# Kernel optimization log

Measured on AMD Instinct MI355X. Metric: run time of the kernel, lower is better.

## Reference

```python
import jax, jax.numpy as jnp
import numpy as np

N = 10000      # nodes
E = 320000     # edges (before self-loops)
IN = 128       # input features
HID = 32       # hidden channels per head
HEADS = 8
OUT = 40       # classes
NEG_SLOPE = 0.2  # PyG GATConv leaky_relu slope


def gat_conv(x, W, a_src, a_dst, b, src, dst, n, concat):
    """One PyG-style GATConv (eval mode, self-loops already in src/dst)."""
    H, C = a_src.shape
    xp = (x @ W).reshape(n, H, C)                       # [N,H,C]
    al_s = jnp.einsum('nhc,hc->nh', xp, a_src)          # [N,H]
    al_d = jnp.einsum('nhc,hc->nh', xp, a_dst)          # [N,H]
    e = jax.nn.leaky_relu(al_s[src] + al_d[dst], NEG_SLOPE)  # [E,H]
    # segment softmax over incoming edges of each dst node
    m = jax.ops.segment_max(e, dst, num_segments=n)
    ee = jnp.exp(e - m[dst])
    s = jax.ops.segment_sum(ee, dst, num_segments=n)
    alpha = ee / (s[dst] + 1e-16)                       # [E,H]
    out = jax.ops.segment_sum(alpha[:, :, None] * xp[src], dst, num_segments=n)  # [N,H,C]
    out = out.reshape(n, H * C) if concat else out.mean(axis=1)
    return out + b


def setup_inputs() -> dict:
    key = jax.random.key(0)
    ks = jax.random.split(key, 16)
    p = lambda k, shape: (jax.random.normal(k, shape, jnp.float32) * 0.1)
    HC = HEADS * HID
    return {
        'x': jax.random.normal(ks[0], (N, IN), jnp.float32),
        'edge_index': jax.random.randint(ks[1], (2, E), 0, N),
        'W1': p(ks[2], (IN, HC)), 'a_src1': p(ks[3], (HEADS, HID)), 'a_dst1': p(ks[4], (HEADS, HID)), 'b1': jnp.zeros((HC,), jnp.float32),
        'W2': p(ks[5], (HC, HC)), 'a_src2': p(ks[6], (HEADS, HID)), 'a_dst2': p(ks[7], (HEADS, HID)), 'b2': jnp.zeros((HC,), jnp.float32),
        'W3': p(ks[8], (HC, OUT)), 'a_src3': p(ks[9], (1, OUT)), 'a_dst3': p(ks[10], (1, OUT)), 'b3': jnp.zeros((OUT,), jnp.float32),
    }


def reference(x, edge_index, W1, a_src1, a_dst1, b1, W2, a_src2, a_dst2, b2,
              W3, a_src3, a_dst3, b3):
    n = x.shape[0]
    loop = jnp.arange(n, dtype=edge_index.dtype)
    src = jnp.concatenate([edge_index[0], loop])   # PyG add_self_loops=True
    dst = jnp.concatenate([edge_index[1], loop])
    h = jax.nn.elu(gat_conv(x, W1, a_src1, a_dst1, b1, src, dst, n, True))
    h = jax.nn.elu(gat_conv(h, W2, a_src2, a_dst2, b2, src, dst, n, True))
    h = gat_conv(h, W3, a_src3, a_dst3, b3, src, dst, n, False)
    return jax.nn.log_softmax(h, axis=1)
```

## Files before the change

kernel.cpp:

```cpp
#include <hip/hip_runtime.h>
#include <hip/hip_bf16.h>
#include <math.h>


#define DEV_INLINE __device__ __forceinline__

typedef __attribute__((ext_vector_type(8))) short short8;
typedef __attribute__((ext_vector_type(4))) float f32x4;
typedef unsigned short ushort_t;
typedef unsigned int uint_t;

#define ELLW 128

DEV_INLINE float leaky02(float x) { return x > 0.f ? x : 0.2f * x; }
DEV_INLINE float elu1(float x) { return x > 0.f ? x : expm1f(x); }

DEV_INLINE ushort_t f2bf(float f) {
    uint_t u = __float_as_uint(f);
    u += 0x7FFFu + ((u >> 16) & 1u);
    return (ushort_t)(u >> 16);
}
DEV_INLINE float bf2f(ushort_t u) { return __uint_as_float(((uint_t)u) << 16); }


DEV_INLINE void prep_body(int i,
                          const float* __restrict__ x, ushort_t* __restrict__ x_bf,
                          const float* __restrict__ W1, ushort_t* __restrict__ W1T,
                          const float* __restrict__ W2, ushort_t* __restrict__ W2T,
                          const float* __restrict__ W3, ushort_t* __restrict__ W3T,
                          const float* __restrict__ as1, const float* __restrict__ ad1,
                          const float* __restrict__ as2, const float* __restrict__ ad2,
                          const float* __restrict__ as3, const float* __restrict__ ad3,
                          int n) {
    int xcnt = n * 32;
    if (i < xcnt) {
        float4 v = *(const float4*)(x + (size_t)i * 4);
        ushort4 o;
        o.x = f2bf(v.x); o.y = f2bf(v.y); o.z = f2bf(v.z); o.w = f2bf(v.w);
        *(ushort4*)(x_bf + (size_t)i * 4) = o;
        return;
    }
    i -= xcnt;
    if (i < 128 * 256) {
        int k = i >> 8, c = i & 255;
        W1T[(size_t)c * 128 + k] = f2bf(W1[i]);
        return;
    }
    i -= 128 * 256;
    if (i < 256 * 256) {
        int k = i >> 8, c = i & 255;
        W2T[(size_t)c * 256 + k] = f2bf(W2[i]);
        return;
    }
    i -= 256 * 256;
    if (i < 256 * 40) {
        int k = i / 40, c = i - k * 40;
        W3T[(size_t)c * 256 + k] = f2bf(W3[i]);
        return;
    }
    i -= 256 * 40;
    if (i < 1024) {
        int h = i >> 7, k = i & 127;
        float acc = 0.f;
#pragma unroll
        for (int c = 0; c < 32; ++c) acc += W1[k * 256 + h * 32 + c] * as1[h * 32 + c];
        W1T[(size_t)(256 + h) * 128 + k] = f2bf(acc);
        return;
    }
    i -= 1024;
    if (i < 1024) {
        int h = i >> 7, k = i & 127;
        float acc = 0.f;
#pragma unroll
        for (int c = 0; c < 32; ++c) acc += W1[k * 256 + h * 32 + c] * ad1[h * 32 + c];
        W1T[(size_t)(264 + h) * 128 + k] = f2bf(acc);
        return;
    }
    i -= 1024;
    if (i < 2048) {
        int h = i >> 8, k = i & 255;
        float acc = 0.f;
#pragma unroll
        for (int c = 0; c < 32; ++c) acc += W2[k * 256 + h * 32 + c] * as2[h * 32 + c];
        W2T[(size_t)(256 + h) * 256 + k] = f2bf(acc);
        return;
    }
    i -= 2048;
    if (i < 2048) {
        int h = i >> 8, k = i & 255;
        float acc = 0.f;
#pragma unroll
        for (int c = 0; c < 32; ++c) acc += W2[k * 256 + h * 32 + c] * ad2[h * 32 + c];
        W2T[(size_t)(264 + h) * 256 + k] = f2bf(acc);
        return;
    }
    i -= 2048;
    if (i < 256) {
        float acc = 0.f;
#pragma unroll
        for (int c = 0; c < 40; ++c) acc += W3[i * 40 + c] * as3[c];
        W3T[(size_t)40 * 256 + i] = f2bf(acc);
        return;
    }
    i -= 256;
    if (i < 256) {
        float acc = 0.f;
#pragma unroll
        for (int c = 0; c < 40; ++c) acc += W3[i * 40 + c] * ad3[c];
        W3T[(size_t)41 * 256 + i] = f2bf(acc);
        return;
    }
}

__global__ void prep_scatter_kernel(const float* __restrict__ x, ushort_t* __restrict__ x_bf,
                                    const float* __restrict__ W1, ushort_t* __restrict__ W1T,
                                    const float* __restrict__ W2, ushort_t* __restrict__ W2T,
                                    const float* __restrict__ W3, ushort_t* __restrict__ W3T,
                                    const float* __restrict__ as1, const float* __restrict__ ad1,
                                    const float* __restrict__ as2, const float* __restrict__ ad2,
                                    const float* __restrict__ as3, const float* __restrict__ ad3,
                                    const int* __restrict__ src, const int* __restrict__ dst,
                                    int* __restrict__ cursor, int* __restrict__ ell,
                                    int e, int scatBlocks, int n) {
    if (blockIdx.x < scatBlocks) {
        int i4 = (blockIdx.x * blockDim.x + threadIdx.x) * 4;
        if (i4 + 3 < e) {
            int4 d = *(const int4*)(dst + i4);
            int4 s = *(const int4*)(src + i4);
            int p;
            p = atomicAdd(&cursor[d.x], 1); ell[d.x * ELLW + p] = s.x;
            p = atomicAdd(&cursor[d.y], 1); ell[d.y * ELLW + p] = s.y;
            p = atomicAdd(&cursor[d.z], 1); ell[d.z * ELLW + p] = s.z;
            p = atomicAdd(&cursor[d.w], 1); ell[d.w * ELLW + p] = s.w;
        } else {
            for (int k = i4; k < e; ++k) {
                int p = atomicAdd(&cursor[dst[k]], 1);
                ell[dst[k] * ELLW + p] = src[k];
            }
        }
        return;
    }
    int i = (blockIdx.x - scatBlocks) * blockDim.x + threadIdx.x;
    prep_body(i, x, x_bf, W1, W1T, W2, W2T, W3, W3T, as1, ad1, as2, ad2, as3, ad3, n);
}


DEV_INLINE int lds_slot(int r, int c) { return r * 4 + ((c + (r >> 1)) & 3); }

DEV_INLINE void gemm_body(const ushort_t* __restrict__ A, const ushort_t* __restrict__ BT,
                          ushort_t* __restrict__ C, float* __restrict__ ALS,
                          float* __restrict__ ALD, int M, int NOUT, int NH, int NTOT,
                          int K, int bx, int by) {
    __shared__ ushort_t As[64 * 32];
    __shared__ ushort_t Bs[64 * 32];
    const int tid = threadIdx.x;
    const int wave = tid >> 6, lane = tid & 63;
    const int row0 = by * 64;
    const int col0 = bx * 64;

    const int sr = tid >> 2, sc = tid & 3;
    const int a_row = row0 + sr;
    const int b_row = col0 + sr;

    const int fr = lane & 15;
    const int fc = lane >> 4;

    f32x4 acc0 = {}, acc1 = {}, acc2 = {}, acc3 = {};

    for (int k0 = 0; k0 < K; k0 += 32) {
        short8 av = {}, bv = {};
        if (a_row < M) av = *(const short8*)(A + (size_t)a_row * K + k0 + sc * 8);
        if (b_row < NTOT) bv = *(const short8*)(BT + (size_t)b_row * K + k0 + sc * 8);
        __syncthreads();
        *(short8*)(As + lds_slot(sr, sc) * 8) = av;
        *(short8*)(Bs + lds_slot(sr, sc) * 8) = bv;
        __syncthreads();

        const int arow = wave * 16 + fr;
        short8 afrag = *(const short8*)(As + lds_slot(arow, fc) * 8);
        short8 b0 = *(const short8*)(Bs + lds_slot(0 * 16 + fr, fc) * 8);
        short8 b1 = *(const short8*)(Bs + lds_slot(1 * 16 + fr, fc) * 8);
        short8 b2 = *(const short8*)(Bs + lds_slot(2 * 16 + fr, fc) * 8);
        short8 b3 = *(const short8*)(Bs + lds_slot(3 * 16 + fr, fc) * 8);
        acc0 = __builtin_amdgcn_mfma_f32_16x16x32_bf16(afrag, b0, acc0, 0, 0, 0);
        acc1 = __builtin_amdgcn_mfma_f32_16x16x32_bf16(afrag, b1, acc1, 0, 0, 0);
        acc2 = __builtin_amdgcn_mfma_f32_16x16x32_bf16(afrag, b2, acc2, 0, 0, 0);
        acc3 = __builtin_amdgcn_mfma_f32_16x16x32_bf16(afrag, b3, acc3, 0, 0, 0);
    }

    const int crow = row0 + wave * 16 + (lane >> 4) * 4;
    const int ccol = col0 + (lane & 15);
    f32x4 accs[4] = {acc0, acc1, acc2, acc3};
#pragma unroll
    for (int ct = 0; ct < 4; ++ct) {
        int col = ccol + ct * 16;
#pragma unroll
        for (int j = 0; j < 4; ++j) {
            int row = crow + j;
            if (row >= M) continue;
            float v = accs[ct][j];
            if (col < NOUT) {
                C[(size_t)row * NOUT + col] = f2bf(v);
            } else {
                int cc = col - NOUT;
                if (cc < NH) ALS[(size_t)row * NH + cc] = v;
                else if (cc < 2 * NH) ALD[(size_t)row * NH + (cc - NH)] = v;
            }
        }
    }
}

__global__ __launch_bounds__(256) void gemm_kernel(const ushort_t* __restrict__ A,
                                                   const ushort_t* __restrict__ BT,
                                                   ushort_t* __restrict__ C,
                                                   float* __restrict__ ALS,
                                                   float* __restrict__ ALD,
                                                   int M, int NOUT, int NH, int NTOT,
                                                   int K, int gx) {
    gemm_body(A, BT, C, ALS, ALD, M, NOUT, NH, NTOT, K, blockIdx.x % gx, blockIdx.x / gx);
}


__global__ __launch_bounds__(256) void aggregate_h8_kernel(const ushort_t* __restrict__ xp,
                                                           const float* __restrict__ als,
                                                           const float* __restrict__ ald,
                                                           const int* __restrict__ degv,
                                                           const int* __restrict__ ell,
                                                           const float* __restrict__ bias,
                                                           ushort_t* __restrict__ out, int n) {
    int node = (blockIdx.x * blockDim.x + threadIdx.x) >> 6;
    int lane = threadIdx.x & 63;
    if (node >= n) return;
    const int half = lane >> 5;
    const int lh = lane & 31;
    const int ch = lh * 8;
    const int head = lh >> 2;
    const int deg = degv[node];
    const int rs = node * ELLW, re = rs + deg;
    const float ad = ald[node * 8 + head];
    const float m = leaky02(als[node * 8 + head] + ad);

    float acc[8];
    float ssum;
    if (half == 0) {
        short8 sv = *(const short8*)(xp + (size_t)node * 256 + ch);
#pragma unroll
        for (int i = 0; i < 8; ++i) acc[i] = bf2f((ushort_t)sv[i]);
        ssum = 1.0f;
    } else {
#pragma unroll
        for (int i = 0; i < 8; ++i) acc[i] = 0.f;
        ssum = 0.f;
    }

    for (int base = rs; base < re; base += 64) {
        const int cnt = (re - base < 64) ? (re - base) : 64;
        int myi = (lane < cnt) ? ell[base + lane] : 0;
        int j = 0;
        for (; j + 8 <= cnt; j += 8) {
            int s0 = __shfl(myi, j + half);
            int s1 = __shfl(myi, j + 2 + half);
            int s2 = __shfl(myi, j + 4 + half);
            int s3 = __shfl(myi, j + 6 + half);
            float a0 = als[s0 * 8 + head];
            float a1 = als[s1 * 8 + head];
            float a2 = als[s2 * 8 + head];
            float a3 = als[s3 * 8 + head];
            short8 v0 = *(const short8*)(xp + (size_t)s0 * 256 + ch);
            short8 v1 = *(const short8*)(xp + (size_t)s1 * 256 + ch);
            short8 v2 = *(const short8*)(xp + (size_t)s2 * 256 + ch);
            short8 v3 = *(const short8*)(xp + (size_t)s3 * 256 + ch);
            float p0 = __expf(leaky02(a0 + ad) - m);
            float p1 = __expf(leaky02(a1 + ad) - m);
            float p2 = __expf(leaky02(a2 + ad) - m);
            float p3 = __expf(leaky02(a3 + ad) - m);
            ssum += (p0 + p1) + (p2 + p3);
#pragma unroll
            for (int i = 0; i < 8; ++i)
                acc[i] += (p0 * bf2f((ushort_t)v0[i]) + p1 * bf2f((ushort_t)v1[i]))
                        + (p2 * bf2f((ushort_t)v2[i]) + p3 * bf2f((ushort_t)v3[i]));
        }
        for (; j < cnt; j += 2) {
            int jj = j + half;
            int s = __shfl(myi, jj & 63);
            bool valid = jj < cnt;
            float a = als[s * 8 + head];
            short8 v = *(const short8*)(xp + (size_t)s * 256 + ch);
            float p = valid ? __expf(leaky02(a + ad) - m) : 0.f;
            ssum += p;
#pragma unroll
            for (int i = 0; i < 8; ++i) acc[i] += p * bf2f((ushort_t)v[i]);
        }
    }

    ssum += __shfl_xor(ssum, 32);
#pragma unroll
    for (int i = 0; i < 8; ++i) acc[i] += __shfl_xor(acc[i], 32);

    if (half == 0) {
        float inv = 1.f / ssum;
        float4 ba = *(const float4*)(bias + ch);
        float4 bb = *(const float4*)(bias + ch + 4);
        float bv[8] = {ba.x, ba.y, ba.z, ba.w, bb.x, bb.y, bb.z, bb.w};
        short8 o;
#pragma unroll
        for (int i = 0; i < 8; ++i) o[i] = (short)f2bf(elu1(acc[i] * inv + bv[i]));
        *(short8*)(out + (size_t)node * 256 + ch) = o;
    }
}


__global__ __launch_bounds__(256) void aggregate_out_kernel(const ushort_t* __restrict__ xp,
                                                            const float* __restrict__ als,
                                                            const float* __restrict__ ald,
                                                            const int* __restrict__ degv,
                                                            const int* __restrict__ ell,
                                                            const float* __restrict__ bias,
                                                            float* __restrict__ out, int n) {
    int node = (blockIdx.x * blockDim.x + threadIdx.x) >> 6;
    int lane = threadIdx.x & 63;
    if (node >= n) return;
    const int half = lane >> 5;
    const int lh = lane & 31;
    const bool act = lh < 20;
    const int ch = lh * 2;
    const int deg = degv[node];
    const int rs = node * ELLW, re = rs + deg;
    const float ad = ald[node];
    const float m = leaky02(als[node] + ad);

    float a0, a1, ssum;
    if (half == 0) {
        if (act) {
            ushort2 sv = *(const ushort2*)(xp + (size_t)node * 40 + ch);
            a0 = bf2f(sv.x); a1 = bf2f(sv.y);
        } else { a0 = a1 = 0.f; }
        ssum = 1.0f;
    } else { a0 = a1 = 0.f; ssum = 0.f; }

    for (int base = rs; base < re; base += 64) {
        const int cnt = (re - base < 64) ? (re - base) : 64;
        int myi = (lane < cnt) ? ell[base + lane] : 0;
        int j = 0;
        for (; j + 8 <= cnt; j += 8) {
            int s0 = __shfl(myi, j + half);
            int s1 = __shfl(myi, j + 2 + half);
            int s2 = __shfl(myi, j + 4 + half);
            int s3 = __shfl(myi, j + 6 + half);
            float e0 = als[s0];
            float e1 = als[s1];
            float e2 = als[s2];
            float e3 = als[s3];
            ushort2 v0 = act ? *(const ushort2*)(xp + (size_t)s0 * 40 + ch) : ushort2{0, 0};
            ushort2 v1 = act ? *(const ushort2*)(xp + (size_t)s1 * 40 + ch) : ushort2{0, 0};
            ushort2 v2 = act ? *(const ushort2*)(xp + (size_t)s2 * 40 + ch) : ushort2{0, 0};
            ushort2 v3 = act ? *(const ushort2*)(xp + (size_t)s3 * 40 + ch) : ushort2{0, 0};
            float p0 = __expf(leaky02(e0 + ad) - m);
            float p1 = __expf(leaky02(e1 + ad) - m);
            float p2 = __expf(leaky02(e2 + ad) - m);
            float p3 = __expf(leaky02(e3 + ad) - m);
            ssum += (p0 + p1) + (p2 + p3);
            a0 += (p0 * bf2f(v0.x) + p1 * bf2f(v1.x)) + (p2 * bf2f(v2.x) + p3 * bf2f(v3.x));
            a1 += (p0 * bf2f(v0.y) + p1 * bf2f(v1.y)) + (p2 * bf2f(v2.y) + p3 * bf2f(v3.y));
        }
        for (; j < cnt; j += 2) {
            int jj = j + half;
            int s = __shfl(myi, jj & 63);
            bool valid = jj < cnt;
            float a = als[s];
            ushort2 v = act ? *(const ushort2*)(xp + (size_t)s * 40 + ch) : ushort2{0, 0};
            float p = valid ? __expf(leaky02(a + ad) - m) : 0.f;
            ssum += p;
            a0 += p * bf2f(v.x);
            a1 += p * bf2f(v.y);
        }
    }

    ssum += __shfl_xor(ssum, 32);
    a0 += __shfl_xor(a0, 32);
    a1 += __shfl_xor(a1, 32);

    float inv = 1.f / ssum;
    float2 b2 = act ? *(const float2*)(bias + ch) : float2{0.f, 0.f};
    float o0 = act ? (a0 * inv + b2.x) : -INFINITY;
    float o1 = act ? (a1 * inv + b2.y) : -INFINITY;

    float mx = fmaxf(o0, o1);
#pragma unroll
    for (int off = 16; off >= 1; off >>= 1) mx = fmaxf(mx, __shfl_xor(mx, off));
    float ex = act ? (__expf(o0 - mx) + __expf(o1 - mx)) : 0.f;
#pragma unroll
    for (int off = 16; off >= 1; off >>= 1) ex += __shfl_xor(ex, off);
    float lse = mx + __logf(ex);
    if (half == 0 && act) {
        float2 o = {o0 - lse, o1 - lse};
        *(float2*)(out + (size_t)node * 40 + ch) = o;
    }
}


extern "C" void kernel_launch(void* const* d_in, const int* in_sizes, int n_in,
                              void* d_out, int out_size, void* d_ws, size_t ws_size,
                              hipStream_t stream) {
    const float* x      = (const float*)d_in[0];
    const int*   edge   = (const int*)d_in[1];
    const float* W1     = (const float*)d_in[2];
    const float* a_src1 = (const float*)d_in[3];
    const float* a_dst1 = (const float*)d_in[4];
    const float* b1     = (const float*)d_in[5];
    const float* W2     = (const float*)d_in[6];
    const float* a_src2 = (const float*)d_in[7];
    const float* a_dst2 = (const float*)d_in[8];
    const float* b2     = (const float*)d_in[9];
    const float* W3     = (const float*)d_in[10];
    const float* a_src3 = (const float*)d_in[11];
    const float* a_dst3 = (const float*)d_in[12];
    const float* b3     = (const float*)d_in[13];
    float* out = (float*)d_out;

    const int n = in_sizes[0] / 128;
    const int e = in_sizes[1] / 2;

    char* ws = (char*)d_ws;
    size_t off = 0;
    auto alloc = [&](size_t bytes) -> void* {
        void* p = ws + off;
        off += (bytes + 255) & ~(size_t)255;
        return p;
    };
    ushort_t* xp        = (ushort_t*)alloc((size_t)n * 256 * 2);
    ushort_t* h_bf      = (ushort_t*)alloc((size_t)n * 256 * 2);
    ushort_t* xp3       = (ushort_t*)alloc((size_t)n * 40 * 2);
    ushort_t* x_bf      = (ushort_t*)alloc((size_t)n * 128 * 2);
    ushort_t* W1T       = (ushort_t*)alloc((size_t)272 * 128 * 2);
    ushort_t* W2T       = (ushort_t*)alloc((size_t)272 * 256 * 2);
    ushort_t* W3T       = (ushort_t*)alloc((size_t)42 * 256 * 2);
    float*    als       = (float*)alloc((size_t)n * 8 * 4);
    float*    ald       = (float*)alloc((size_t)n * 8 * 4);
    int*      cursor    = (int*)alloc((size_t)n * 4);
    int*      ell       = (int*)alloc((size_t)n * ELLW * 4);
    (void)ws_size;

    const int* srcs = edge;
    const int* dsts = edge + e;

    const int mby = (n + 63) / 64;
    const int e4blocks = ((e + 3) / 4 + 255) / 256;

    hipMemsetAsync(cursor, 0, (size_t)n * 4, stream);
    {
        int prep_total = n * 32 + 128 * 256 + 256 * 256 + 256 * 40
                       + 1024 + 1024 + 2048 + 2048 + 256 + 256;
        int prepBlocks = (prep_total + 255) / 256;
        prep_scatter_kernel<<<e4blocks + prepBlocks, 256, 0, stream>>>(
            x, x_bf, W1, W1T, W2, W2T, W3, W3T,
            a_src1, a_dst1, a_src2, a_dst2, a_src3, a_dst3,
            srcs, dsts, cursor, ell, e, e4blocks, n);
    }

    const int agg_grid = (n * 64 + 255) / 256;

    gemm_kernel<<<5 * mby, 256, 0, stream>>>(x_bf, W1T, xp, als, ald, n, 256, 8, 272, 128, 5);
    aggregate_h8_kernel<<<agg_grid, 256, 0, stream>>>(xp, als, ald, cursor, ell, b1, h_bf, n);
    gemm_kernel<<<5 * mby, 256, 0, stream>>>(h_bf, W2T, xp, als, ald, n, 256, 8, 272, 256, 5);
    aggregate_h8_kernel<<<agg_grid, 256, 0, stream>>>(xp, als, ald, cursor, ell, b2, h_bf, n);
    gemm_kernel<<<1 * mby, 256, 0, stream>>>(h_bf, W3T, xp3, als, ald, n, 40, 1, 42, 256, 1);
    aggregate_out_kernel<<<agg_grid, 256, 0, stream>>>(xp3, als, ald, cursor, ell, b3, out, n);
}
```

Before: 110.1 us.

## Fuse edge scatter with first GEMM and convert x to bf16 inline

Replaces the memset plus the combined prep/scatter kernel with a prep kernel that zeros the cursor and transposes the weights, followed by a kernel that runs the ELL edge scatter and the first-layer GEMM in one grid. The GEMM now reads fp32 x directly and converts it to bf16 while loading, which removes the x_bf intermediate buffer and one launch. The scatter goes from four edges per thread to one edge per thread. Barriers were added after the k-loop because LDS is now passed in as a parameter.

```diff
diff --git a/kernel.cpp b/kernel.cpp
--- a/kernel.cpp
+++ b/kernel.cpp
@@ -23,24 +23,16 @@
 DEV_INLINE float bf2f(ushort_t u) { return __uint_as_float(((uint_t)u) << 16); }
 
 
-DEV_INLINE void prep_body(int i,
-                          const float* __restrict__ x, ushort_t* __restrict__ x_bf,
-                          const float* __restrict__ W1, ushort_t* __restrict__ W1T,
-                          const float* __restrict__ W2, ushort_t* __restrict__ W2T,
-                          const float* __restrict__ W3, ushort_t* __restrict__ W3T,
-                          const float* __restrict__ as1, const float* __restrict__ ad1,
-                          const float* __restrict__ as2, const float* __restrict__ ad2,
-                          const float* __restrict__ as3, const float* __restrict__ ad3,
-                          int n) {
-    int xcnt = n * 32;
-    if (i < xcnt) {
-        float4 v = *(const float4*)(x + (size_t)i * 4);
-        ushort4 o;
-        o.x = f2bf(v.x); o.y = f2bf(v.y); o.z = f2bf(v.z); o.w = f2bf(v.w);
-        *(ushort4*)(x_bf + (size_t)i * 4) = o;
-        return;
-    }
-    i -= xcnt;
+__global__ void prep_kernel(const float* __restrict__ W1, ushort_t* __restrict__ W1T,
+                            const float* __restrict__ W2, ushort_t* __restrict__ W2T,
+                            const float* __restrict__ W3, ushort_t* __restrict__ W3T,
+                            const float* __restrict__ as1, const float* __restrict__ ad1,
+                            const float* __restrict__ as2, const float* __restrict__ ad2,
+                            const float* __restrict__ as3, const float* __restrict__ ad3,
+                            int* __restrict__ cursor, int n) {
+    int i = blockIdx.x * blockDim.x + threadIdx.x;
+    if (i < n) { cursor[i] = 0; return; }
+    i -= n;
     if (i < 128 * 256) {
         int k = i >> 8, c = i & 255;
         W1T[(size_t)c * 128 + k] = f2bf(W1[i]);
@@ -112,47 +104,14 @@
     }
 }
 
-__global__ void prep_scatter_kernel(const float* __restrict__ x, ushort_t* __restrict__ x_bf,
-                                    const float* __restrict__ W1, ushort_t* __restrict__ W1T,
-                                    const float* __restrict__ W2, ushort_t* __restrict__ W2T,
-                                    const float* __restrict__ W3, ushort_t* __restrict__ W3T,
-                                    const float* __restrict__ as1, const float* __restrict__ ad1,
-                                    const float* __restrict__ as2, const float* __restrict__ ad2,
-                                    const float* __restrict__ as3, const float* __restrict__ ad3,
-                                    const int* __restrict__ src, const int* __restrict__ dst,
-                                    int* __restrict__ cursor, int* __restrict__ ell,
-                                    int e, int scatBlocks, int n) {
-    if (blockIdx.x < scatBlocks) {
-        int i4 = (blockIdx.x * blockDim.x + threadIdx.x) * 4;
-        if (i4 + 3 < e) {
-            int4 d = *(const int4*)(dst + i4);
-            int4 s = *(const int4*)(src + i4);
-            int p;
-            p = atomicAdd(&cursor[d.x], 1); ell[d.x * ELLW + p] = s.x;
-            p = atomicAdd(&cursor[d.y], 1); ell[d.y * ELLW + p] = s.y;
-            p = atomicAdd(&cursor[d.z], 1); ell[d.z * ELLW + p] = s.z;
-            p = atomicAdd(&cursor[d.w], 1); ell[d.w * ELLW + p] = s.w;
-        } else {
-            for (int k = i4; k < e; ++k) {
-                int p = atomicAdd(&cursor[dst[k]], 1);
-                ell[dst[k] * ELLW + p] = src[k];
-            }
-        }
-        return;
-    }
-    int i = (blockIdx.x - scatBlocks) * blockDim.x + threadIdx.x;
-    prep_body(i, x, x_bf, W1, W1T, W2, W2T, W3, W3T, as1, ad1, as2, ad2, as3, ad3, n);
-}
-
 
 DEV_INLINE int lds_slot(int r, int c) { return r * 4 + ((c + (r >> 1)) & 3); }
 
-DEV_INLINE void gemm_body(const ushort_t* __restrict__ A, const ushort_t* __restrict__ BT,
+DEV_INLINE void gemm_body(ushort_t* __restrict__ As, ushort_t* __restrict__ Bs,
+                          const ushort_t* __restrict__ A, const ushort_t* __restrict__ BT,
                           ushort_t* __restrict__ C, float* __restrict__ ALS,
                           float* __restrict__ ALD, int M, int NOUT, int NH, int NTOT,
                           int K, int bx, int by) {
-    __shared__ ushort_t As[64 * 32];
-    __shared__ ushort_t Bs[64 * 32];
     const int tid = threadIdx.x;
     const int wave = tid >> 6, lane = tid & 63;
     const int row0 = by * 64;
@@ -187,6 +146,7 @@
         acc2 = __builtin_amdgcn_mfma_f32_16x16x32_bf16(afrag, b2, acc2, 0, 0, 0);
         acc3 = __builtin_amdgcn_mfma_f32_16x16x32_bf16(afrag, b3, acc3, 0, 0, 0);
     }
+    __syncthreads();
 
     const int crow = row0 + wave * 16 + (lane >> 4) * 4;
     const int ccol = col0 + (lane & 15);
@@ -210,6 +170,76 @@
     }
 }
 
+DEV_INLINE void gemm1_body(ushort_t* __restrict__ As, ushort_t* __restrict__ Bs,
+                           const float* __restrict__ X, const ushort_t* __restrict__ BT,
+                           ushort_t* __restrict__ C, float* __restrict__ ALS,
+                           float* __restrict__ ALD, int M, int bx, int by) {
+    const int tid = threadIdx.x;
+    const int wave = tid >> 6, lane = tid & 63;
+    const int row0 = by * 64;
+    const int col0 = bx * 64;
+
+    const int sr = tid >> 2, sc = tid & 3;
+    const int a_row = row0 + sr;
+    const int b_row = col0 + sr;
+
+    const int fr = lane & 15;
+    const int fc = lane >> 4;
+
+    f32x4 acc0 = {}, acc1 = {}, acc2 = {}, acc3 = {};
+
+    for (int k0 = 0; k0 < 128; k0 += 32) {
+        short8 av = {}, bv = {};
+        if (a_row < M) {
+            const float* xp = X + (size_t)a_row * 128 + k0 + sc * 8;
+            float4 f0 = *(const float4*)(xp);
+            float4 f1 = *(const float4*)(xp + 4);
+            av[0] = (short)f2bf(f0.x); av[1] = (short)f2bf(f0.y);
+            av[2] = (short)f2bf(f0.z); av[3] = (short)f2bf(f0.w);
+            av[4] = (short)f2bf(f1.x); av[5] = (short)f2bf(f1.y);
+            av[6] = (short)f2bf(f1.z); av[7] = (short)f2bf(f1.w);
+        }
+        if (b_row < 272) bv = *(const short8*)(BT + (size_t)b_row * 128 + k0 + sc * 8);
+        __syncthreads();
+        *(short8*)(As + lds_slot(sr, sc) * 8) = av;
+        *(short8*)(Bs + lds_slot(sr, sc) * 8) = bv;
+        __syncthreads();
+
+        const int arow = wave * 16 + fr;
+        short8 afrag = *(const short8*)(As + lds_slot(arow, fc) * 8);
+        short8 b0 = *(const short8*)(Bs + lds_slot(0 * 16 + fr, fc) * 8);
+        short8 b1 = *(const short8*)(Bs + lds_slot(1 * 16 + fr, fc) * 8);
+        short8 b2 = *(const short8*)(Bs + lds_slot(2 * 16 + fr, fc) * 8);
+        short8 b3 = *(const short8*)(Bs + lds_slot(3 * 16 + fr, fc) * 8);
+        acc0 = __builtin_amdgcn_mfma_f32_16x16x32_bf16(afrag, b0, acc0, 0, 0, 0);
+        acc1 = __builtin_amdgcn_mfma_f32_16x16x32_bf16(afrag, b1, acc1, 0, 0, 0);
+        acc2 = __builtin_amdgcn_mfma_f32_16x16x32_bf16(afrag, b2, acc2, 0, 0, 0);
+        acc3 = __builtin_amdgcn_mfma_f32_16x16x32_bf16(afrag, b3, acc3, 0, 0, 0);
+    }
+    __syncthreads();
+
+    const int crow = row0 + wave * 16 + (lane >> 4) * 4;
+    const int ccol = col0 + (lane & 15);
+    f32x4 accs[4] = {acc0, acc1, acc2, acc3};
+#pragma unroll
+    for (int ct = 0; ct < 4; ++ct) {
+        int col = ccol + ct * 16;
+#pragma unroll
+        for (int j = 0; j < 4; ++j) {
+            int row = crow + j;
+            if (row >= M) continue;
+            float v = accs[ct][j];
+            if (col < 256) {
+                C[(size_t)row * 256 + col] = f2bf(v);
+            } else {
+                int cc = col - 256;
+                if (cc < 8) ALS[(size_t)row * 8 + cc] = v;
+                else if (cc < 16) ALD[(size_t)row * 8 + (cc - 8)] = v;
+            }
+        }
+    }
+}
+
 __global__ __launch_bounds__(256) void gemm_kernel(const ushort_t* __restrict__ A,
                                                    const ushort_t* __restrict__ BT,
                                                    ushort_t* __restrict__ C,
@@ -217,7 +247,35 @@
                                                    float* __restrict__ ALD,
                                                    int M, int NOUT, int NH, int NTOT,
                                                    int K, int gx) {
-    gemm_body(A, BT, C, ALS, ALD, M, NOUT, NH, NTOT, K, blockIdx.x % gx, blockIdx.x / gx);
+    __shared__ ushort_t As[64 * 32];
+    __shared__ ushort_t Bs[64 * 32];
+    gemm_body(As, Bs, A, BT, C, ALS, ALD, M, NOUT, NH, NTOT, K, blockIdx.x % gx, blockIdx.x / gx);
+}
+
+__global__ __launch_bounds__(256) void scatter_gemm1_kernel(const int* __restrict__ src,
+                                                            const int* __restrict__ dst,
+                                                            int* __restrict__ cursor,
+                                                            int* __restrict__ ell, int e,
+                                                            int svb,
+                                                            const float* __restrict__ X,
+                                                            const ushort_t* __restrict__ BT,
+                                                            ushort_t* __restrict__ C,
+                                                            float* __restrict__ ALS,
+                                                            float* __restrict__ ALD,
+                                                            int M, int gx) {
+    __shared__ ushort_t As[64 * 32];
+    __shared__ ushort_t Bs[64 * 32];
+    if (blockIdx.x < svb) {
+        int i = blockIdx.x * 256 + threadIdx.x;
+        if (i < e) {
+            int d = dst[i];
+            int p = atomicAdd(&cursor[d], 1);
+            ell[d * ELLW + p] = src[i];
+        }
+        return;
+    }
+    int b = blockIdx.x - svb;
+    gemm1_body(As, Bs, X, BT, C, ALS, ALD, M, b % gx, b / gx);
 }
 
 
@@ -431,7 +489,6 @@
     ushort_t* xp        = (ushort_t*)alloc((size_t)n * 256 * 2);
     ushort_t* h_bf      = (ushort_t*)alloc((size_t)n * 256 * 2);
     ushort_t* xp3       = (ushort_t*)alloc((size_t)n * 40 * 2);
-    ushort_t* x_bf      = (ushort_t*)alloc((size_t)n * 128 * 2);
     ushort_t* W1T       = (ushort_t*)alloc((size_t)272 * 128 * 2);
     ushort_t* W2T       = (ushort_t*)alloc((size_t)272 * 256 * 2);
     ushort_t* W3T       = (ushort_t*)alloc((size_t)42 * 256 * 2);
@@ -445,22 +502,20 @@
     const int* dsts = edge + e;
 
     const int mby = (n + 63) / 64;
-    const int e4blocks = ((e + 3) / 4 + 255) / 256;
-
-    hipMemsetAsync(cursor, 0, (size_t)n * 4, stream);
+    const int svb = (e + 255) / 256;
+
     {
-        int prep_total = n * 32 + 128 * 256 + 256 * 256 + 256 * 40
+        int prep_total = n + 128 * 256 + 256 * 256 + 256 * 40
                        + 1024 + 1024 + 2048 + 2048 + 256 + 256;
-        int prepBlocks = (prep_total + 255) / 256;
-        prep_scatter_kernel<<<e4blocks + prepBlocks, 256, 0, stream>>>(
-            x, x_bf, W1, W1T, W2, W2T, W3, W3T,
-            a_src1, a_dst1, a_src2, a_dst2, a_src3, a_dst3,
-            srcs, dsts, cursor, ell, e, e4blocks, n);
-    }
+        prep_kernel<<<(prep_total + 255) / 256, 256, 0, stream>>>(
+            W1, W1T, W2, W2T, W3, W3T,
+            a_src1, a_dst1, a_src2, a_dst2, a_src3, a_dst3, cursor, n);
+    }
+    scatter_gemm1_kernel<<<svb + 5 * mby, 256, 0, stream>>>(
+        srcs, dsts, cursor, ell, e, svb, x, W1T, xp, als, ald, n, 5);
 
     const int agg_grid = (n * 64 + 255) / 256;
 
-    gemm_kernel<<<5 * mby, 256, 0, stream>>>(x_bf, W1T, xp, als, ald, n, 256, 8, 272, 128, 5);
     aggregate_h8_kernel<<<agg_grid, 256, 0, stream>>>(xp, als, ald, cursor, ell, b1, h_bf, n);
     gemm_kernel<<<5 * mby, 256, 0, stream>>>(h_bf, W2T, xp, als, ald, n, 256, 8, 272, 256, 5);
     aggregate_h8_kernel<<<agg_grid, 256, 0, stream>>>(xp, als, ald, cursor, ell, b2, h_bf, n);
```

After: 106.0 us. -3.7%, faster.
